# Optimization experiments

Measured on AMD Instinct MI355X. Metric: run time of the kernel, lower is better.

The kernel has to match this reference:

```python
import math
import jax, jax.numpy as jnp
import numpy as np

N_HEADS = 8
EMB = 512
BATCH = 256
NKEYS = 2048
NEG_INF = -jnp.inf


def setup_inputs() -> dict:
    key = jax.random.key(0)
    kq, kk, kv, kw, km = jax.random.split(key, 5)
    query = jax.random.normal(kq, (BATCH, 1, EMB), dtype=jnp.float32)
    keys = jax.random.normal(kk, (BATCH, NKEYS, EMB), dtype=jnp.float32)
    value = jax.random.normal(kv, (BATCH, NKEYS, EMB), dtype=jnp.float32)
    W_o = jax.random.normal(kw, (EMB, EMB), dtype=jnp.float32) / math.sqrt(EMB)
    mask = jax.random.randint(km, (BATCH, 1, NKEYS), 0, 2) == 1  # bool [B,1,K]
    return {"query": query, "key": keys, "value": value, "W_o": W_o, "mask": mask}


def _make_heads(v):
    # [B, N, D] -> [H, B, N, D/H]
    b, n, d = v.shape
    return v.reshape(b, n, N_HEADS, d // N_HEADS).transpose(2, 0, 1, 3)


def reference(query, key, value, W_o, mask):
    qh = _make_heads(query)            # [H, B, 1, dh]
    kh = _make_heads(key)              # [H, B, K, dh]
    vh = _make_heads(value)            # [H, B, K, dh]
    dh = qh.shape[-1]
    # scaled dot-product scores: [H, B, 1, K]
    u = jnp.einsum("hbqd,hbkd->hbqk", qh, kh) / math.sqrt(dh)
    # boolean masking: mask [B,1,K] broadcasts over heads
    logits = jnp.where(mask[None], NEG_INF, u)
    a = jax.nn.softmax(logits, axis=-1)            # [H, B, 1, K]
    oh = jnp.einsum("hbqk,hbkd->hbqd", a, vh)      # [H, B, 1, dh]
    # unmake heads: [H,B,1,dh] -> [B,1,H*dh]
    b = oh.shape[1]
    merged = oh.transpose(1, 2, 0, 3).reshape(b, 1, N_HEADS * dh)
    out = merged @ W_o.T                           # Linear, no bias
    return out
```

## Files before the change

kernel.cpp:

```cpp
#include <hip/hip_runtime.h>


#define NB    256
#define NK    2048
#define EMBD  512
#define NH    8
#define DH    64
#define SCP   2052
#define ACP   520

__device__ __forceinline__ void barrier_lgkm() {
    asm volatile("s_waitcnt lgkmcnt(0)" ::: "memory");
    __builtin_amdgcn_s_barrier();
}

__device__ __forceinline__ float4 ld4(const float* p) {
    return *reinterpret_cast<const float4*>(p);
}

__global__ __launch_bounds__(1024) void attn_kernel(
    const float* __restrict__ q,
    const float* __restrict__ kptr,
    const float* __restrict__ vptr,
    const int* __restrict__ mask,
    float* __restrict__ merged)
{
    const int b    = blockIdx.x;
    const int t    = threadIdx.x;
    const int w    = t >> 6;
    const int lane = t & 63;
    const int hq   = lane >> 3;
    const int sub  = lane & 7;

    __shared__ float sc[NH][SCP];
    __shared__ int   smask[NK];
    __shared__ float redm[16], redl[16];

    const float* qb = q + (size_t)b * EMBD + lane * 8;
    const float4 qa = ld4(qb);
    const float4 qc = ld4(qb + 4);
    const float* kb = kptr + (size_t)b * NK * EMBD + lane * 8;
    const float* vb = vptr + (size_t)b * NK * EMBD + lane * 8;
    const int*   mrow = mask + (size_t)b * NK;

    #pragma unroll 2
    for (int it = 0; it < NK / 16; ++it) {
        const int key = it * 16 + w;
        const int mk  = mrow[key];
        if (lane == 0) smask[key] = mk;
        if (mk) {
            if (sub == 0) sc[hq][key] = -1e30f;
        } else {
            const float* kk = kb + (size_t)key * EMBD;
            const float4 ka = ld4(kk);
            const float4 kc = ld4(kk + 4);
            float s = qa.x * ka.x + qa.y * ka.y + qa.z * ka.z + qa.w * ka.w
                    + qc.x * kc.x + qc.y * kc.y + qc.z * kc.z + qc.w * kc.w;
            s += __shfl_xor(s, 1, 8);
            s += __shfl_xor(s, 2, 8);
            s += __shfl_xor(s, 4, 8);
            if (sub == 0) sc[hq][key] = s * 0.125f;
        }
    }

    const int hh = w >> 1;
    const int tl = ((w & 1) << 6) | lane;

    barrier_lgkm();

    float lm = -INFINITY;
    #pragma unroll
    for (int j = 0; j < 16; ++j) lm = fmaxf(lm, sc[hh][j * 128 + tl]);
    #pragma unroll
    for (int off = 32; off >= 1; off >>= 1)
        lm = fmaxf(lm, __shfl_xor(lm, off, 64));
    if (lane == 0) redm[w] = lm;
    barrier_lgkm();
    const float m = fmaxf(redm[hh * 2], redm[hh * 2 + 1]);

    float ls = 0.f;
    #pragma unroll
    for (int j = 0; j < 16; ++j) {
        const int kk2 = j * 128 + tl;
        const float p = __expf(sc[hh][kk2] - m);
        sc[hh][kk2] = p;
        ls += p;
    }
    #pragma unroll
    for (int off = 32; off >= 1; off >>= 1) ls += __shfl_xor(ls, off, 64);
    if (lane == 0) redl[w] = ls;
    barrier_lgkm();

    float4 a0 = {0.f, 0.f, 0.f, 0.f};
    float4 a1 = {0.f, 0.f, 0.f, 0.f};
    #pragma unroll 2
    for (int it = 0; it < NK / 16; ++it) {
        const int key = it * 16 + w;
        if (!smask[key]) {
            const float* vv = vb + (size_t)key * EMBD;
            const float4 va = ld4(vv);
            const float4 vc = ld4(vv + 4);
            const float p = sc[hq][key];
            a0.x = fmaf(p, va.x, a0.x); a0.y = fmaf(p, va.y, a0.y);
            a0.z = fmaf(p, va.z, a0.z); a0.w = fmaf(p, va.w, a0.w);
            a1.x = fmaf(p, vc.x, a1.x); a1.y = fmaf(p, vc.y, a1.y);
            a1.z = fmaf(p, vc.z, a1.z); a1.w = fmaf(p, vc.w, a1.w);
        }
    }

    barrier_lgkm();
    float* accb = &sc[0][0];
    *reinterpret_cast<float4*>(&accb[w * ACP + lane * 8])     = a0;
    *reinterpret_cast<float4*>(&accb[w * ACP + lane * 8 + 4]) = a1;
    barrier_lgkm();

    if (t < EMBD) {
        float s = 0.f;
        #pragma unroll
        for (int ww = 0; ww < 16; ++ww) s += accb[ww * ACP + t];
        const int h = t >> 6;
        const float den = redl[h * 2] + redl[h * 2 + 1];
        merged[(size_t)b * EMBD + t] = s / den;
    }
}

__global__ __launch_bounds__(256) void proj_kernel_split(
    const float* __restrict__ merged,
    const float* __restrict__ Wo,
    float* __restrict__ out)
{
    const int bt = blockIdx.x >> 3;
    const int jt = blockIdx.x & 7;
    const int t  = threadIdx.x;
    __shared__ float4 mrow[8 * 128];
    #pragma unroll
    for (int k = 0; k < 4; ++k) {
        const int idx = k * 256 + t;
        mrow[idx] = reinterpret_cast<const float4*>(
            merged + (size_t)bt * 8 * EMBD)[idx];
    }
    __syncthreads();

    const int j    = jt * 64 + (t & 63);
    const int brel = t >> 6;
    const float4* wrow = reinterpret_cast<const float4*>(Wo + (size_t)j * EMBD);
    const float4* m0 = &mrow[brel * 128];
    const float4* m1 = &mrow[(brel + 4) * 128];
    float s0 = 0.f, s1 = 0.f;
    #pragma unroll 4
    for (int i = 0; i < 128; ++i) {
        const float4 wv = wrow[i];
        const float4 x0 = m0[i];
        const float4 x1 = m1[i];
        s0 += wv.x * x0.x + wv.y * x0.y + wv.z * x0.z + wv.w * x0.w;
        s1 += wv.x * x1.x + wv.y * x1.y + wv.z * x1.z + wv.w * x1.w;
    }
    out[(size_t)(bt * 8 + brel) * EMBD + j] = s0;
    out[(size_t)(bt * 8 + brel + 4) * EMBD + j] = s1;
}

__global__ __launch_bounds__(256) void proj_kernel_inplace(
    const float* __restrict__ merged,
    const float* __restrict__ Wo,
    float* __restrict__ out)
{
    const int b = blockIdx.x;
    const int t = threadIdx.x;
    __shared__ float mrow[EMBD];
    *reinterpret_cast<float2*>(&mrow[t * 2]) =
        *reinterpret_cast<const float2*>(&merged[(size_t)b * EMBD + t * 2]);
    __syncthreads();

    const float4* mv = reinterpret_cast<const float4*>(mrow);
    #pragma unroll
    for (int half = 0; half < 2; ++half) {
        const int j = t + half * 256;
        const float4* wrow = reinterpret_cast<const float4*>(Wo + (size_t)j * EMBD);
        float s = 0.f;
        #pragma unroll 4
        for (int i = 0; i < EMBD / 4; ++i) {
            const float4 wv = wrow[i];
            const float4 qv = mv[i];
            s += wv.x * qv.x + wv.y * qv.y + wv.z * qv.z + wv.w * qv.w;
        }
        out[(size_t)b * EMBD + j] = s;
    }
}

extern "C" void kernel_launch(void* const* d_in, const int* in_sizes, int n_in,
                              void* d_out, int out_size, void* d_ws, size_t ws_size,
                              hipStream_t stream) {
    const float* q    = (const float*)d_in[0];
    const float* kptr = (const float*)d_in[1];
    const float* vptr = (const float*)d_in[2];
    const float* Wo   = (const float*)d_in[3];
    const int*   mask = (const int*)d_in[4];
    float* out = (float*)d_out;

    float* merged = (ws_size >= (size_t)NB * EMBD * sizeof(float))
                        ? (float*)d_ws : out;

    attn_kernel<<<NB, 1024, 0, stream>>>(q, kptr, vptr, mask, merged);
    if (merged != out)
        proj_kernel_split<<<NB, 256, 0, stream>>>(merged, Wo, out);
    else
        proj_kernel_inplace<<<NB, 256, 0, stream>>>(merged, Wo, out);
}
```

Baseline: 259.4 us.

## Compact unmasked keys into a shared list and iterate only over them

Builds a compacted list of unmasked key indices per batch row with wave ballots and a prefix sum over per-wave counts. It pre-fills the score buffer with the masked value. Both the QK and PV loops then walk only the live keys, spread evenly across the 16 waves, with the next key index prefetched. This removes per-key mask branches and the load imbalance across waves. The cost is extra barriers, an LDS fill pass, and a dependent LDS read before each global load.

```diff
diff --git a/kernel.cpp b/kernel.cpp
--- a/kernel.cpp
+++ b/kernel.cpp
@@ -33,7 +33,8 @@
     const int sub  = lane & 7;
 
     __shared__ float sc[NH][SCP];
-    __shared__ int   smask[NK];
+    __shared__ int   klist[NK];
+    __shared__ int   wavecnt[16];
     __shared__ float redm[16], redl[16];
 
     const float* qb = q + (size_t)b * EMBD + lane * 8;
@@ -43,23 +44,49 @@
     const float* vb = vptr + (size_t)b * NK * EMBD + lane * 8;
     const int*   mrow = mask + (size_t)b * NK;
 
-    #pragma unroll 2
-    for (int it = 0; it < NK / 16; ++it) {
-        const int key = it * 16 + w;
-        const int mk  = mrow[key];
-        if (lane == 0) smask[key] = mk;
-        if (mk) {
-            if (sub == 0) sc[hq][key] = -1e30f;
-        } else {
+    const int kA = w * 128 + lane;
+    const int kB = kA + 64;
+    const int mA = mrow[kA];
+    const int mB = mrow[kB];
+    const unsigned long long balA = __ballot(mA == 0);
+    const unsigned long long balB = __ballot(mB == 0);
+    if (lane == 0) wavecnt[w] = __popcll(balA) + __popcll(balB);
+    float4* scf = reinterpret_cast<float4*>(&sc[0][0]);
+    #pragma unroll
+    for (int i = 0; i < 5; ++i) {
+        const int idx = i * 1024 + t;
+        if (idx < (NH * SCP) / 4)
+            scf[idx] = make_float4(-1e30f, -1e30f, -1e30f, -1e30f);
+    }
+    barrier_lgkm();
+
+    int off = 0, nun = 0;
+    #pragma unroll
+    for (int i = 0; i < 16; ++i) {
+        const int c = wavecnt[i];
+        off += (i < w) ? c : 0;
+        nun += c;
+    }
+    const unsigned long long below = (1ull << lane) - 1ull;
+    if (!mA) klist[off + __popcll(balA & below)] = kA;
+    if (!mB) klist[off + __popcll(balA) + __popcll(balB & below)] = kB;
+    barrier_lgkm();
+
+    {
+        int key = (w < nun) ? klist[w] : 0;
+        for (int slot = w; slot < nun; slot += 16) {
+            const int nslot = slot + 16;
+            const int nkey = (nslot < nun) ? klist[nslot] : 0;
             const float* kk = kb + (size_t)key * EMBD;
             const float4 ka = ld4(kk);
             const float4 kc = ld4(kk + 4);
-            float s = qa.x * ka.x + qa.y * ka.y + qa.z * ka.z + qa.w * ka.w
-                    + qc.x * kc.x + qc.y * kc.y + qc.z * kc.z + qc.w * kc.w;
-            s += __shfl_xor(s, 1, 8);
-            s += __shfl_xor(s, 2, 8);
-            s += __shfl_xor(s, 4, 8);
-            if (sub == 0) sc[hq][key] = s * 0.125f;
+            float sv = qa.x * ka.x + qa.y * ka.y + qa.z * ka.z + qa.w * ka.w
+                     + qc.x * kc.x + qc.y * kc.y + qc.z * kc.z + qc.w * kc.w;
+            sv += __shfl_xor(sv, 1, 8);
+            sv += __shfl_xor(sv, 2, 8);
+            sv += __shfl_xor(sv, 4, 8);
+            if (sub == 0) sc[hq][key] = sv * 0.125f;
+            key = nkey;
         }
     }
 
@@ -72,8 +99,8 @@
     #pragma unroll
     for (int j = 0; j < 16; ++j) lm = fmaxf(lm, sc[hh][j * 128 + tl]);
     #pragma unroll
-    for (int off = 32; off >= 1; off >>= 1)
-        lm = fmaxf(lm, __shfl_xor(lm, off, 64));
+    for (int offr = 32; offr >= 1; offr >>= 1)
+        lm = fmaxf(lm, __shfl_xor(lm, offr, 64));
     if (lane == 0) redm[w] = lm;
     barrier_lgkm();
     const float m = fmaxf(redm[hh * 2], redm[hh * 2 + 1]);
@@ -87,16 +114,17 @@
         ls += p;
     }
     #pragma unroll
-    for (int off = 32; off >= 1; off >>= 1) ls += __shfl_xor(ls, off, 64);
+    for (int offr = 32; offr >= 1; offr >>= 1) ls += __shfl_xor(ls, offr, 64);
     if (lane == 0) redl[w] = ls;
     barrier_lgkm();
 
     float4 a0 = {0.f, 0.f, 0.f, 0.f};
     float4 a1 = {0.f, 0.f, 0.f, 0.f};
-    #pragma unroll 2
-    for (int it = 0; it < NK / 16; ++it) {
-        const int key = it * 16 + w;
-        if (!smask[key]) {
+    {
+        int key = (w < nun) ? klist[w] : 0;
+        for (int slot = w; slot < nun; slot += 16) {
+            const int nslot = slot + 16;
+            const int nkey = (nslot < nun) ? klist[nslot] : 0;
             const float* vv = vb + (size_t)key * EMBD;
             const float4 va = ld4(vv);
             const float4 vc = ld4(vv + 4);
@@ -105,6 +133,7 @@
             a0.z = fmaf(p, va.z, a0.z); a0.w = fmaf(p, va.w, a0.w);
             a1.x = fmaf(p, vc.x, a1.x); a1.y = fmaf(p, vc.y, a1.y);
             a1.z = fmaf(p, vc.z, a1.z); a1.w = fmaf(p, vc.w, a1.w);
+            key = nkey;
         }
     }
 
```

After: 208.3 us. -19.7%, faster.
